# Kernel tuning notes

Measured on AMD Instinct MI355X. Metric: run time of the kernel, lower is better.

## Reference

```python
import jax, jax.numpy as jnp
import numpy as np

B, H, W, CIN, COUT, KH, KW = 8, 256, 256, 64, 64, 3, 3

def setup_inputs() -> dict:
    key = jax.random.key(0)
    k1, k2 = jax.random.split(key)
    inputs = jax.random.normal(k1, (B, H, W, CIN), dtype=jnp.float32)
    kernel = jax.random.normal(k2, (CIN, COUT, KH, KW), dtype=jnp.float32)
    return {"inputs": inputs, "kernel": kernel}

def reference(inputs, kernel):
    # Stride-1 transposed convolution with 'full' output size:
    # out[b, p, q, co] = sum_{ci,i,j} inputs[b, i, j, ci] * kernel[ci, co, p-i, q-j]
    # which is a full (mathematical) convolution. lax performs cross-correlation,
    # so flip the kernel spatially and pad by (k-1) on each side.
    kh, kw = kernel.shape[2], kernel.shape[3]
    k_flipped = jnp.flip(kernel, axis=(2, 3))
    out = jax.lax.conv_general_dilated(
        inputs, k_flipped,
        window_strides=(1, 1),
        padding=[(kh - 1, kh - 1), (kw - 1, kw - 1)],
        dimension_numbers=("NHWC", "IOHW", "NHWC"))
    # out: [B, H+KH-1, W+KW-1, COUT]; original call() adds no bias.
    return out
```

## Files before the change

kernel.cpp:

```cpp
#include <hip/hip_runtime.h>
#include <hip/hip_bf16.h>


#define OH 258
#define OW 258

typedef __bf16 bf16x8 __attribute__((ext_vector_type(8)));
typedef float  f32x4  __attribute__((ext_vector_type(4)));

__global__ void prep_w_kernel(const float* __restrict__ k, __bf16* __restrict__ wsW) {
    int i = blockIdx.x * 256 + threadIdx.x;
    int j  = i & 7;
    int ml = (i >> 3) & 15;
    int h  = (i >> 7) & 3;
    int nt = (i >> 9) & 3;
    int st = i >> 11;
    int s  = st & 1, tap = st >> 1;
    int ci = s * 32 + h * 8 + j;
    int co = nt * 16 + ml;
    wsW[i] = (__bf16)k[ci * 576 + co * 9 + tap];
}

__device__ __forceinline__ void tile_coords(int tau, int& b, int& p0, int& q0) {
    int bb = tau / 153;
    int rr = tau - bb * 153;
    int py = rr / 17;
    b  = bb;
    p0 = py * 32;
    q0 = (rr - py * 17) * 16;
}

__device__ __forceinline__ void issue_patch_loads(
        const float* __restrict__ in, int b, int p0, int q0, int tid,
        f32x4 (&v0)[5], f32x4 (&v1)[5]) {
    #pragma unroll
    for (int k = 0; k < 5; ++k) {
        const int it = tid + k * 1024;
        const bool act = (k < 4) || (tid < 800);
        int pix = it >> 3, c8 = it & 7;
        int r = pix / 18, c = pix - r * 18;
        int ip = p0 - 2 + r, iq = q0 - 2 + c;
        f32x4 z = {0.f, 0.f, 0.f, 0.f};
        v0[k] = z; v1[k] = z;
        if (act && (unsigned)ip < 256u && (unsigned)iq < 256u) {
            const float* g = in + (((size_t)b * 256 + ip) * 256 + iq) * 64 + c8 * 8;
            v0[k] = *(const f32x4*)g;
            v1[k] = *(const f32x4*)(g + 4);
        }
    }
}

__global__ __launch_bounds__(1024, 4)
void tconv_kernel(const float* __restrict__ in, const __bf16* __restrict__ wsW,
                  float* __restrict__ out) {
    __shared__ __bf16 lds_in[612 * 64];
    __shared__ __bf16 lds_w[36864];

    const int tid = threadIdx.x;

    #pragma unroll
    for (int k = 0; k < 5; ++k) {
        const int g = tid + k * 1024;
        if ((k < 4) || (tid < 512))
            *(bf16x8*)&lds_w[(size_t)g * 8] = *(const bf16x8*)&wsW[(size_t)g * 8];
    }

    const int wv = tid >> 6, lane = tid & 63;
    const int ml = lane & 15, h = lane >> 4;
    const int woff = h * 128 + ml * 8;
    const int rbase = wv * 2;

    const int bx = blockIdx.x;
    const int n_t = (bx < 200) ? 5 : 4;

    int cb, cp0, cq0;
    tile_coords(bx, cb, cp0, cq0);
    f32x4 v0[5], v1[5];
    issue_patch_loads(in, cb, cp0, cq0, tid, v0, v1);

    int nb = 0, np0 = 0, nq0 = 0;

    #pragma unroll 1
    for (int t = 0; t < n_t; ++t) {
        asm volatile("" ::: "memory");
        __builtin_amdgcn_s_barrier();

        #pragma unroll
        for (int k = 0; k < 5; ++k) {
            const int it = tid + k * 1024;
            if ((k < 4) || (tid < 800)) {
                int pix = it >> 3, c8 = it & 7;
                bf16x8 w;
                w[0]=(__bf16)v0[k][0]; w[1]=(__bf16)v0[k][1];
                w[2]=(__bf16)v0[k][2]; w[3]=(__bf16)v0[k][3];
                w[4]=(__bf16)v1[k][0]; w[5]=(__bf16)v1[k][1];
                w[6]=(__bf16)v1[k][2]; w[7]=(__bf16)v1[k][3];
                *(bf16x8*)&lds_in[pix * 64 + ((c8 ^ (pix & 7)) * 8)] = w;
            }
        }
        if (t + 1 < n_t) {
            tile_coords(bx + (t + 1) * 256, nb, np0, nq0);
            issue_patch_loads(in, nb, np0, nq0, tid, v0, v1);
        }
        asm volatile("s_waitcnt lgkmcnt(0)" ::: "memory");
        __builtin_amdgcn_s_barrier();

        f32x4 acc[2][4] = {};
        #pragma unroll 3
        for (int tap = 0; tap < 9; ++tap) {
            const int kh = tap / 3, kw = tap - kh * 3;
            const __bf16* wt = lds_w + tap * 4096;
            #pragma unroll
            for (int s = 0; s < 2; ++s) {
                bf16x8 bfr[4];
                #pragma unroll
                for (int nt = 0; nt < 4; ++nt)
                    bfr[nt] = *(const bf16x8*)(wt + s * 2048 + nt * 512 + woff);
                const int j = s * 4 + h;
                #pragma unroll
                for (int mt = 0; mt < 2; ++mt) {
                    int row = rbase + mt + 2 - kh;
                    int pix = row * 18 + (2 - kw) + ml;
                    bf16x8 afr = *(const bf16x8*)&lds_in[pix * 64 + ((j ^ (pix & 7)) * 8)];
                    #pragma unroll
                    for (int nt = 0; nt < 4; ++nt)
                        acc[mt][nt] = __builtin_amdgcn_mfma_f32_16x16x32_bf16(
                            bfr[nt], afr, acc[mt][nt], 0, 0, 0);
                }
            }
        }

        const int q = cq0 + ml;
        #pragma unroll
        for (int mt = 0; mt < 2; ++mt) {
            int p = cp0 + rbase + mt;
            if (p < OH && q < OW) {
                float* op = out + (((size_t)cb * OH + p) * OW + q) * 64 + h * 4;
                #pragma unroll
                for (int nt = 0; nt < 4; ++nt)
                    *(f32x4*)(op + nt * 16) = acc[mt][nt];
            }
        }
        cb = nb; cp0 = np0; cq0 = nq0;
    }
}

extern "C" void kernel_launch(void* const* d_in, const int* in_sizes, int n_in,
                              void* d_out, int out_size, void* d_ws, size_t ws_size,
                              hipStream_t stream) {
    (void)in_sizes; (void)n_in; (void)out_size; (void)ws_size;
    const float* in   = (const float*)d_in[0];
    const float* kern = (const float*)d_in[1];
    float* out = (float*)d_out;
    __bf16* wsW = (__bf16*)d_ws;

    prep_w_kernel<<<144, 256, 0, stream>>>(kern, wsW);
    tconv_kernel<<<256, 1024, 0, stream>>>(in, wsW, out);
}
```

Before: 252.9 us.

## Double-buffer input patch in LDS and stream weights from global memory

Replaces the single LDS input buffer plus LDS weight copy with two input patch buffers, so the next tile is written to LDS midway through the current tile's MFMA work instead of before it. This removes one barrier per tile and overlaps the LDS commit with compute. Weights are now read straight from global/L2 with software double-buffered register prefetch, which frees LDS but adds global load latency and traffic inside the inner MFMA loop. The global load for tile t+2 is issued during tile t.

```diff
diff --git a/kernel.cpp b/kernel.cpp
--- a/kernel.cpp
+++ b/kernel.cpp
@@ -50,85 +50,105 @@
     }
 }
 
+__device__ __forceinline__ void commit_patch(
+        __bf16* __restrict__ dst, int tid,
+        const f32x4 (&v0)[5], const f32x4 (&v1)[5]) {
+    #pragma unroll
+    for (int k = 0; k < 5; ++k) {
+        const int it = tid + k * 1024;
+        if ((k < 4) || (tid < 800)) {
+            int pix = it >> 3, c8 = it & 7;
+            bf16x8 w;
+            w[0]=(__bf16)v0[k][0]; w[1]=(__bf16)v0[k][1];
+            w[2]=(__bf16)v0[k][2]; w[3]=(__bf16)v0[k][3];
+            w[4]=(__bf16)v1[k][0]; w[5]=(__bf16)v1[k][1];
+            w[6]=(__bf16)v1[k][2]; w[7]=(__bf16)v1[k][3];
+            *(bf16x8*)&dst[pix * 64 + ((c8 ^ (pix & 7)) * 8)] = w;
+        }
+    }
+}
+
+template<int G0, int G1>
+__device__ __forceinline__ void compute_span(
+        const __bf16* __restrict__ cur, const __bf16* __restrict__ wsW,
+        int woff, int rbase, int ml, int h, f32x4 (&acc)[2][4]) {
+    bf16x8 wb[2][4];
+    #pragma unroll
+    for (int nt = 0; nt < 4; ++nt)
+        wb[G0 & 1][nt] = *(const bf16x8*)(wsW + G0 * 2048 + nt * 512 + woff);
+    #pragma unroll
+    for (int g = G0; g < G1; ++g) {
+        if (g + 1 < G1) {
+            #pragma unroll
+            for (int nt = 0; nt < 4; ++nt)
+                wb[(g + 1) & 1][nt] =
+                    *(const bf16x8*)(wsW + (g + 1) * 2048 + nt * 512 + woff);
+        }
+        const int tap = g >> 1, s = g & 1;
+        const int kh = tap / 3, kw = tap - kh * 3;
+        const int j = s * 4 + h;
+        #pragma unroll
+        for (int mt = 0; mt < 2; ++mt) {
+            int row = rbase + mt + 2 - kh;
+            int pix = row * 18 + (2 - kw) + ml;
+            bf16x8 afr = *(const bf16x8*)&cur[pix * 64 + ((j ^ (pix & 7)) * 8)];
+            #pragma unroll
+            for (int nt = 0; nt < 4; ++nt)
+                acc[mt][nt] = __builtin_amdgcn_mfma_f32_16x16x32_bf16(
+                    wb[g & 1][nt], afr, acc[mt][nt], 0, 0, 0);
+        }
+    }
+}
+
 __global__ __launch_bounds__(1024, 4)
 void tconv_kernel(const float* __restrict__ in, const __bf16* __restrict__ wsW,
                   float* __restrict__ out) {
-    __shared__ __bf16 lds_in[612 * 64];
-    __shared__ __bf16 lds_w[36864];
+    __shared__ __bf16 lds_a[612 * 64];
+    __shared__ __bf16 lds_b[612 * 64];
 
     const int tid = threadIdx.x;
-
-    #pragma unroll
-    for (int k = 0; k < 5; ++k) {
-        const int g = tid + k * 1024;
-        if ((k < 4) || (tid < 512))
-            *(bf16x8*)&lds_w[(size_t)g * 8] = *(const bf16x8*)&wsW[(size_t)g * 8];
-    }
+    const int bx = blockIdx.x;
+    const int n_t = (bx < 200) ? 5 : 4;
 
     const int wv = tid >> 6, lane = tid & 63;
     const int ml = lane & 15, h = lane >> 4;
     const int woff = h * 128 + ml * 8;
     const int rbase = wv * 2;
 
-    const int bx = blockIdx.x;
-    const int n_t = (bx < 200) ? 5 : 4;
+    int cb, cp0, cq0;
+    f32x4 v0[5], v1[5];
 
-    int cb, cp0, cq0;
     tile_coords(bx, cb, cp0, cq0);
-    f32x4 v0[5], v1[5];
     issue_patch_loads(in, cb, cp0, cq0, tid, v0, v1);
-
-    int nb = 0, np0 = 0, nq0 = 0;
+    commit_patch(lds_a, tid, v0, v1);
+    if (n_t > 1) {
+        int nb, np0, nq0;
+        tile_coords(bx + 256, nb, np0, nq0);
+        issue_patch_loads(in, nb, np0, nq0, tid, v0, v1);
+    }
+    asm volatile("s_waitcnt lgkmcnt(0)" ::: "memory");
+    __builtin_amdgcn_s_barrier();
 
     #pragma unroll 1
     for (int t = 0; t < n_t; ++t) {
-        asm volatile("" ::: "memory");
-        __builtin_amdgcn_s_barrier();
+        __bf16* cur = (t & 1) ? lds_b : lds_a;
+        __bf16* nxt = (t & 1) ? lds_a : lds_b;
+        tile_coords(bx + t * 256, cb, cp0, cq0);
 
-        #pragma unroll
-        for (int k = 0; k < 5; ++k) {
-            const int it = tid + k * 1024;
-            if ((k < 4) || (tid < 800)) {
-                int pix = it >> 3, c8 = it & 7;
-                bf16x8 w;
-                w[0]=(__bf16)v0[k][0]; w[1]=(__bf16)v0[k][1];
-                w[2]=(__bf16)v0[k][2]; w[3]=(__bf16)v0[k][3];
-                w[4]=(__bf16)v1[k][0]; w[5]=(__bf16)v1[k][1];
-                w[6]=(__bf16)v1[k][2]; w[7]=(__bf16)v1[k][3];
-                *(bf16x8*)&lds_in[pix * 64 + ((c8 ^ (pix & 7)) * 8)] = w;
+        f32x4 acc[2][4] = {};
+
+        compute_span<0, 9>(cur, wsW, woff, rbase, ml, h, acc);
+
+        if (t + 1 < n_t) {
+            commit_patch(nxt, tid, v0, v1);
+            if (t + 2 < n_t) {
+                int nb, np0, nq0;
+                tile_coords(bx + (t + 2) * 256, nb, np0, nq0);
+                issue_patch_loads(in, nb, np0, nq0, tid, v0, v1);
             }
         }
-        if (t + 1 < n_t) {
-            tile_coords(bx + (t + 1) * 256, nb, np0, nq0);
-            issue_patch_loads(in, nb, np0, nq0, tid, v0, v1);
-        }
-        asm volatile("s_waitcnt lgkmcnt(0)" ::: "memory");
-        __builtin_amdgcn_s_barrier();
 
-        f32x4 acc[2][4] = {};
-        #pragma unroll 3
-        for (int tap = 0; tap < 9; ++tap) {
-            const int kh = tap / 3, kw = tap - kh * 3;
-            const __bf16* wt = lds_w + tap * 4096;
-            #pragma unroll
-            for (int s = 0; s < 2; ++s) {
-                bf16x8 bfr[4];
-                #pragma unroll
-                for (int nt = 0; nt < 4; ++nt)
-                    bfr[nt] = *(const bf16x8*)(wt + s * 2048 + nt * 512 + woff);
-                const int j = s * 4 + h;
-                #pragma unroll
-                for (int mt = 0; mt < 2; ++mt) {
-                    int row = rbase + mt + 2 - kh;
-                    int pix = row * 18 + (2 - kw) + ml;
-                    bf16x8 afr = *(const bf16x8*)&lds_in[pix * 64 + ((j ^ (pix & 7)) * 8)];
-                    #pragma unroll
-                    for (int nt = 0; nt < 4; ++nt)
-                        acc[mt][nt] = __builtin_amdgcn_mfma_f32_16x16x32_bf16(
-                            bfr[nt], afr, acc[mt][nt], 0, 0, 0);
-                }
-            }
-        }
+        compute_span<9, 18>(cur, wsW, woff, rbase, ml, h, acc);
 
         const int q = cq0 + ml;
         #pragma unroll
@@ -141,7 +161,9 @@
                     *(f32x4*)(op + nt * 16) = acc[mt][nt];
             }
         }
-        cb = nb; cp0 = np0; cq0 = nq0;
+
+        asm volatile("s_waitcnt lgkmcnt(0)" ::: "memory");
+        __builtin_amdgcn_s_barrier();
     }
 }
 
```

After: 791.8 us. +213.1%, slower.
